# Kernel optimization log

Measured on AMD Instinct MI355X. Metric: run time of the kernel, lower is better.

## Reference

```python
import jax, jax.numpy as jnp
import numpy as np

SIGMA = 32.0
EPS = 1e-8

def setup_inputs() -> dict:
    key = jax.random.key(0)
    k1, k2, k3 = jax.random.split(key, 3)
    N, D, O = 8192, 512, 512
    x = jax.random.normal(k1, (N, D), dtype=jnp.float32)
    # Linear params (kaiming-normal-ish init represented as scaled normals)
    W = jax.random.normal(k2, (O, D), dtype=jnp.float32) * (2.0 / D) ** 0.5
    b = jnp.zeros((O,), dtype=jnp.float32)
    return {"x": x, "W": W, "b": b}

def reference(x, W, b):
    # squared pairwise L2 distances via the Gram trick: ||xi||^2 + ||xj||^2 - 2 xi.xj
    sq = jnp.sum(x * x, axis=-1)                      # [N]
    sqd = sq[:, None] + sq[None, :] - 2.0 * (x @ x.T)  # [N, N]
    sqd = jnp.maximum(sqd, 0.0)                        # numerical clamp (cdist >= 0)
    weights = jnp.exp(-sqd / (2.0 * SIGMA * SIGMA))    # Gaussian kernel [N, N]
    weights = weights / (jnp.sum(weights, axis=1, keepdims=True) + EPS)
    output = weights @ x                               # Nadaraya-Watson weighted avg [N, D]
    return output @ W.T + b                            # linear head [N, O]
```

## Files before the change

kernel.cpp:

```cpp
#include <hip/hip_runtime.h>
#include <stdint.h>

#define NPTS 8192
#define DIM  512
#define ODIM 512

typedef __attribute__((ext_vector_type(8))) short short8;
typedef __attribute__((ext_vector_type(4))) float f32x4;

__device__ __forceinline__ void gload_lds16(const void* g, void* l) {
  __builtin_amdgcn_global_load_lds(
      (__attribute__((address_space(1))) void*)g,
      (__attribute__((address_space(3))) void*)l, 16, 0, 0);
}

__device__ __forceinline__ short f2bf(float f) {
  uint32_t u = __float_as_uint(f);
  u = (u + 0x7FFFu + ((u >> 16) & 1u)) >> 16;
  return (short)u;
}

__device__ __forceinline__ void gemm256_2ph(const short* __restrict__ A,
                                            const short* __restrict__ B,
                                            int K, int lda, int ldb,
                                            short* lds, f32x4 acc[8][4]) {
  const int tid  = threadIdx.x;
  const int wid  = tid >> 6;
  const int lane = tid & 63;
  const int wr = wid >> 2, wc = wid & 3;
  const int fr = lane & 15, fg = lane >> 4;
  const int srow = lane >> 3;
  const int scol = (lane & 7) << 3;

  const short* sa[4];
  const short* sb[4];
  int da[4];
#pragma unroll
  for (int q = 0; q < 4; ++q) {
    const int gi = q * 8 + wid;
    sa[q] = A + (size_t)(gi * 8 + srow) * lda + scol;
    sb[q] = B + (size_t)(gi * 8 + srow) * ldb + scol;
    da[q] = gi * 512;
  }

  auto stage = [&](int bo, int k0) {
#pragma unroll
    for (int q = 0; q < 4; ++q) gload_lds16(sa[q] + k0, lds + bo + da[q]);
#pragma unroll
    for (int q = 0; q < 4; ++q) gload_lds16(sb[q] + k0, lds + bo + 16384 + da[q]);
  };

  auto compute = [&](int bo) {
    const short* sA = lds + bo;
    const short* sB = lds + bo + 16384;
#pragma unroll
    for (int kk = 0; kk < 2; ++kk) {
      short8 af[8], bb[4];
#pragma unroll
      for (int m = 0; m < 8; ++m)
        af[m] = *(const short8*)(sA + (wr * 128 + m * 16 + fr) * 64 + kk * 32 + fg * 8);
#pragma unroll
      for (int n = 0; n < 4; ++n)
        bb[n] = *(const short8*)(sB + (wc * 64 + n * 16 + fr) * 64 + kk * 32 + fg * 8);
#pragma unroll
      for (int m = 0; m < 8; ++m)
#pragma unroll
        for (int n = 0; n < 4; ++n)
          acc[m][n] = __builtin_amdgcn_mfma_f32_16x16x32_bf16(af[m], bb[n], acc[m][n], 0, 0, 0);
    }
  };

  stage(0, 0);
  __syncthreads();
  int bo = 0;
  const int nt = K >> 6;
  for (int t = 0; t < nt - 1; ++t) {
    stage(bo ^ 32768, (t + 1) << 6);
    compute(bo);
    __syncthreads();
    bo ^= 32768;
  }
  compute(bo);
}

#define ZERO_ACC8(acc)                       \
  {                                          \
    f32x4 _z = {0.f, 0.f, 0.f, 0.f};         \
    _Pragma("unroll")                        \
    for (int m = 0; m < 8; ++m)              \
      _Pragma("unroll")                      \
      for (int n = 0; n < 4; ++n) acc[m][n] = _z; \
  }

__device__ __forceinline__ void gemm_core_nt(const short* __restrict__ A,
                                             const short* __restrict__ B,
                                             int K, int lda, int ldb,
                                             short* smem, f32x4 acc[4][4]) {
  const int tid  = threadIdx.x;
  const int wid  = tid >> 6;
  const int lane = tid & 63;
  const int wr = wid >> 1, wc = wid & 1;
  const int sr = lane >> 2;
  const int sc = (lane & 3) << 3;
  const int fr = lane & 15, fg = lane >> 4;
  short* sA = smem;
  short* sB = smem + 4096;
  short* dA0 = sA + wid * 512;
  short* dA1 = sA + 2048 + wid * 512;
  short* dB0 = sB + wid * 512;
  short* dB1 = sB + 2048 + wid * 512;
  const short* pa0 = A + (size_t)(wid * 16 + sr) * lda + sc;
  const short* pa1 = A + (size_t)(64 + wid * 16 + sr) * lda + sc;
  const short* pb0 = B + (size_t)(wid * 16 + sr) * ldb + sc;
  const short* pb1 = B + (size_t)(64 + wid * 16 + sr) * ldb + sc;

  for (int k0 = 0; k0 < K; k0 += 32) {
    gload_lds16(pa0 + k0, dA0);
    gload_lds16(pa1 + k0, dA1);
    gload_lds16(pb0 + k0, dB0);
    gload_lds16(pb1 + k0, dB1);
    __syncthreads();
    short8 af[4], bb[4];
#pragma unroll
    for (int m = 0; m < 4; ++m)
      af[m] = *(const short8*)(sA + (wr * 64 + m * 16 + fr) * 32 + fg * 8);
#pragma unroll
    for (int n = 0; n < 4; ++n)
      bb[n] = *(const short8*)(sB + (wc * 64 + n * 16 + fr) * 32 + fg * 8);
#pragma unroll
    for (int m = 0; m < 4; ++m)
#pragma unroll
      for (int n = 0; n < 4; ++n)
        acc[m][n] = __builtin_amdgcn_mfma_f32_16x16x32_bf16(af[m], bb[n], acc[m][n], 0, 0, 0);
    __syncthreads();
  }
}

#define ZERO_ACC4(acc)                       \
  {                                          \
    f32x4 _z = {0.f, 0.f, 0.f, 0.f};         \
    _Pragma("unroll")                        \
    for (int m = 0; m < 4; ++m)              \
      _Pragma("unroll")                      \
      for (int n = 0; n < 4; ++n) acc[m][n] = _z; \
  }

__global__ __launch_bounds__(256) void k_prep_x(const float* __restrict__ x,
                                                short* __restrict__ xb,
                                                float* __restrict__ sq) {
  const int row  = blockIdx.x * 4 + (threadIdx.x >> 6);
  const int lane = threadIdx.x & 63;
  const float* px = x + (size_t)row * DIM + lane * 8;
  const float4 v0 = *(const float4*)px;
  const float4 v1 = *(const float4*)(px + 4);
  float s = v0.x*v0.x + v0.y*v0.y + v0.z*v0.z + v0.w*v0.w +
            v1.x*v1.x + v1.y*v1.y + v1.z*v1.z + v1.w*v1.w;
  short8 o;
  o[0]=f2bf(v0.x); o[1]=f2bf(v0.y); o[2]=f2bf(v0.z); o[3]=f2bf(v0.w);
  o[4]=f2bf(v1.x); o[5]=f2bf(v1.y); o[6]=f2bf(v1.z); o[7]=f2bf(v1.w);
  *(short8*)(xb + (size_t)row * DIM + lane * 8) = o;
#pragma unroll
  for (int m = 32; m >= 1; m >>= 1) s += __shfl_xor(s, m);
  if (lane == 0) sq[row] = s;
}

__global__ __launch_bounds__(256) void k_prep_w(const float* __restrict__ W,
                                                short* __restrict__ Wb) {
  const int idx = blockIdx.x * 256 + threadIdx.x;
  const float4 v0 = *(const float4*)(W + (size_t)idx * 8);
  const float4 v1 = *(const float4*)(W + (size_t)idx * 8 + 4);
  short8 o;
  o[0]=f2bf(v0.x); o[1]=f2bf(v0.y); o[2]=f2bf(v0.z); o[3]=f2bf(v0.w);
  o[4]=f2bf(v1.x); o[5]=f2bf(v1.y); o[6]=f2bf(v1.z); o[7]=f2bf(v1.w);
  *(short8*)(Wb + (size_t)idx * 8) = o;
}

__global__ __launch_bounds__(256) void k_ybt(const short* __restrict__ xb,
                                             const short* __restrict__ Wb,
                                             short* __restrict__ YbT) {
  __shared__ short smem[8192];
  f32x4 acc[4][4];
  ZERO_ACC4(acc);
  const int rowBase = blockIdx.y * 128;
  const int colBase = blockIdx.x * 128;
  gemm_core_nt(Wb + (size_t)rowBase * DIM, xb + (size_t)colBase * DIM,
               DIM, DIM, DIM, smem, acc);
  const int lane = threadIdx.x & 63, wid = threadIdx.x >> 6;
  const int wr = wid >> 1, wc = wid & 1, fr = lane & 15, fg = lane >> 4;
#pragma unroll
  for (int m = 0; m < 4; ++m)
#pragma unroll
    for (int n = 0; n < 4; ++n)
#pragma unroll
      for (int r = 0; r < 4; ++r) {
        const int ro = rowBase + wr * 64 + m * 16 + fg * 4 + r;
        const int ci = colBase + wc * 64 + n * 16 + fr;
        YbT[(size_t)ro * NPTS + ci] = f2bf(acc[m][n][r]);
      }
}

__global__ __launch_bounds__(512, 2) void k_pmat(const short* __restrict__ xb,
                                                 const float* __restrict__ sq,
                                                 short* __restrict__ P,
                                                 float* __restrict__ rowsum,
                                                 int jbase, int SW) {
  __shared__ short lds[65536];
  f32x4 acc[8][4];
  ZERO_ACC8(acc);
  const int rowBase = blockIdx.y * 256;
  const int colTile = blockIdx.x * 256;
  const int jglob = jbase + colTile;
  gemm256_2ph(xb + (size_t)rowBase * DIM, xb + (size_t)jglob * DIM,
              DIM, DIM, DIM, lds, acc);
  const int lane = threadIdx.x & 63, wid = threadIdx.x >> 6;
  const int wr = wid >> 2, wc = wid & 3, fr = lane & 15, fg = lane >> 4;
  float sj[4];
#pragma unroll
  for (int n = 0; n < 4; ++n) sj[n] = sq[jglob + wc * 64 + n * 16 + fr];
#pragma unroll
  for (int m = 0; m < 8; ++m) {
#pragma unroll
    for (int r = 0; r < 4; ++r) {
      const int i = rowBase + wr * 128 + m * 16 + fg * 4 + r;
      const float si = sq[i];
      float rs = 0.f;
#pragma unroll
      for (int n = 0; n < 4; ++n) {
        const float t = fminf(2.f * acc[m][n][r] - si - sj[n], 0.f) * (1.0f / 2048.0f);
        const float w = __expf(t);
        rs += w;
        P[(size_t)i * SW + (colTile + wc * 64 + n * 16 + fr)] = f2bf(w);
      }
      rs += __shfl_xor(rs, 1);
      rs += __shfl_xor(rs, 2);
      rs += __shfl_xor(rs, 4);
      rs += __shfl_xor(rs, 8);
      if (fr == 0) atomicAdd(&rowsum[i], rs);
    }
  }
}

__global__ __launch_bounds__(512, 2) void k_pv(const short* __restrict__ P,
                                               const short* __restrict__ YbT,
                                               float* __restrict__ out_acc,
                                               int jbase, int SW, int klen) {
  __shared__ short lds[65536];
  f32x4 acc[8][4];
  ZERO_ACC8(acc);
  const int rowBase = blockIdx.y * 256;
  const int colBase = blockIdx.x * 256;
  const int kz = blockIdx.z * klen;
  gemm256_2ph(P + (size_t)rowBase * SW + kz,
              YbT + (size_t)colBase * NPTS + jbase + kz,
              klen, SW, NPTS, lds, acc);
  const int lane = threadIdx.x & 63, wid = threadIdx.x >> 6;
  const int wr = wid >> 2, wc = wid & 3, fr = lane & 15, fg = lane >> 4;
#pragma unroll
  for (int m = 0; m < 8; ++m)
#pragma unroll
    for (int n = 0; n < 4; ++n)
#pragma unroll
      for (int r = 0; r < 4; ++r) {
        const int i = rowBase + wr * 128 + m * 16 + fg * 4 + r;
        const int o = colBase + wc * 64 + n * 16 + fr;
        atomicAdd(&out_acc[(size_t)i * ODIM + o], acc[m][n][r]);
      }
}

__global__ __launch_bounds__(256) void k_final(const float* __restrict__ out_acc,
                                               const float* __restrict__ rowsum,
                                               const float* __restrict__ bvec,
                                               float* __restrict__ out) {
  const int idx = blockIdx.x * 256 + threadIdx.x;
  const int i = idx >> 7;
  const int o = (idx & 127) << 2;
  const float inv = 1.f / (rowsum[i] + 1e-8f);
  const float4 a = *(const float4*)(out_acc + (size_t)i * ODIM + o);
  const float4 bb = *(const float4*)(bvec + o);
  float4 r;
  r.x = a.x * inv + bb.x;
  r.y = a.y * inv + bb.y;
  r.z = a.z * inv + bb.z;
  r.w = a.w * inv + bb.w;
  *(float4*)(out + (size_t)i * ODIM + o) = r;
}

extern "C" void kernel_launch(void* const* d_in, const int* in_sizes, int n_in,
                              void* d_out, int out_size, void* d_ws, size_t ws_size,
                              hipStream_t stream) {
  (void)in_sizes; (void)n_in; (void)out_size;
  const float* x = (const float*)d_in[0];
  const float* W = (const float*)d_in[1];
  const float* bvec = (const float*)d_in[2];
  float* out = (float*)d_out;
  char* ws = (char*)d_ws;

  short* xb      = (short*)(ws + 0);
  short* Wb      = (short*)(ws + 8388608);
  short* YbT     = (short*)(ws + 8912896);
  float* sq      = (float*)(ws + 17301504);
  float* rowsum  = (float*)(ws + 17334272);
  float* out_acc = (float*)(ws + 17367040);
  short* P       = (short*)(ws + 34144256);

  size_t pav = ws_size > 34144256 ? ws_size - 34144256 : 0;
  int SW = 8192;
  while (SW > 256 && (size_t)NPTS * SW * 2 > pav) SW >>= 1;
  const int nstrips = NPTS / SW;
  int ksplit = SW / 2048;
  if (ksplit < 1) ksplit = 1;
  if (ksplit > 4) ksplit = 4;
  const int klen = SW / ksplit;

  hipMemsetAsync(rowsum, 0, NPTS * sizeof(float), stream);
  hipMemsetAsync(out_acc, 0, (size_t)NPTS * ODIM * sizeof(float), stream);

  k_prep_x<<<dim3(NPTS / 4), 256, 0, stream>>>(x, xb, sq);
  k_prep_w<<<dim3(ODIM * DIM / 8 / 256), 256, 0, stream>>>(W, Wb);
  k_ybt<<<dim3(NPTS / 128, ODIM / 128), 256, 0, stream>>>(xb, Wb, YbT);

  for (int s = 0; s < nstrips; ++s) {
    const int jbase = s * SW;
    k_pmat<<<dim3(SW / 256, NPTS / 256), 512, 0, stream>>>(xb, sq, P, rowsum, jbase, SW);
    k_pv<<<dim3(ODIM / 256, NPTS / 256, ksplit), 512, 0, stream>>>(P, YbT, out_acc, jbase, SW, klen);
  }

  k_final<<<dim3(NPTS * ODIM / 4 / 256), 256, 0, stream>>>(out_acc, rowsum, bvec, out);
}
```

Baseline: 360.5 us.

## Deepen GEMM pipeline to four LDS stages with swizzle and XCD block remap

```diff
diff --git a/kernel.cpp b/kernel.cpp
--- a/kernel.cpp
+++ b/kernel.cpp
@@ -20,67 +20,82 @@
   return (short)u;
 }
 
-__device__ __forceinline__ void gemm256_2ph(const short* __restrict__ A,
-                                            const short* __restrict__ B,
-                                            int K, int lda, int ldb,
-                                            short* lds, f32x4 acc[8][4]) {
-  const int tid  = threadIdx.x;
-  const int wid  = tid >> 6;
-  const int lane = tid & 63;
-  const int wr = wid >> 2, wc = wid & 3;
-  const int fr = lane & 15, fg = lane >> 4;
-  const int srow = lane >> 3;
-  const int scol = (lane & 7) << 3;
-
-  const short* sa[4];
-  const short* sb[4];
-  int da[4];
-#pragma unroll
-  for (int q = 0; q < 4; ++q) {
-    const int gi = q * 8 + wid;
-    sa[q] = A + (size_t)(gi * 8 + srow) * lda + scol;
-    sb[q] = B + (size_t)(gi * 8 + srow) * ldb + scol;
-    da[q] = gi * 512;
-  }
-
-  auto stage = [&](int bo, int k0) {
-#pragma unroll
-    for (int q = 0; q < 4; ++q) gload_lds16(sa[q] + k0, lds + bo + da[q]);
-#pragma unroll
-    for (int q = 0; q < 4; ++q) gload_lds16(sb[q] + k0, lds + bo + 16384 + da[q]);
+#define VMB(N) do {                                          \
+    asm volatile("s_waitcnt vmcnt(" #N ")" ::: "memory");    \
+    __builtin_amdgcn_sched_barrier(0);                       \
+    __builtin_amdgcn_s_barrier();                            \
+    __builtin_amdgcn_sched_barrier(0);                       \
+  } while (0)
+
+#define BARRIER_ONLY() do {                                  \
+    asm volatile("" ::: "memory");                           \
+    __builtin_amdgcn_sched_barrier(0);                       \
+    __builtin_amdgcn_s_barrier();                            \
+    __builtin_amdgcn_sched_barrier(0);                       \
+  } while (0)
+
+__device__ __forceinline__ void gemm256_pipe(const short* __restrict__ A,
+                                             const short* __restrict__ B,
+                                             int K, int lda, int ldb,
+                                             short* lds, f32x4 acc[8][4]) {
+  const int tid = threadIdx.x, wid = tid >> 6, lane = tid & 63;
+  const int wr = wid >> 2, wc = wid & 3, fr = lane & 15, fg = (lane >> 4) & 3;
+  const int nt = K >> 5;
+
+  const short* ga[2]; const short* gb[2]; int dl[2];
+#pragma unroll
+  for (int s = 0; s < 2; ++s) {
+    const int row = (wid * 2 + s) * 16 + (lane >> 2);
+    const int ch  = (lane & 3) ^ ((row & 3) ^ ((row >> 2) & 3));
+    ga[s] = A + (size_t)row * lda + ch * 8;
+    gb[s] = B + (size_t)row * ldb + ch * 8;
+    dl[s] = (wid * 2 + s) * 512;
+  }
+  auto stage = [&](int t) {
+    short* slot = lds + (t & 3) * 16384;
+    const int k0 = t << 5;
+#pragma unroll
+    for (int s = 0; s < 2; ++s) gload_lds16(ga[s] + k0, slot + dl[s]);
+#pragma unroll
+    for (int s = 0; s < 2; ++s) gload_lds16(gb[s] + k0, slot + 8192 + dl[s]);
   };
 
-  auto compute = [&](int bo) {
-    const short* sA = lds + bo;
-    const short* sB = lds + bo + 16384;
-#pragma unroll
-    for (int kk = 0; kk < 2; ++kk) {
-      short8 af[8], bb[4];
-#pragma unroll
-      for (int m = 0; m < 8; ++m)
-        af[m] = *(const short8*)(sA + (wr * 128 + m * 16 + fr) * 64 + kk * 32 + fg * 8);
+  auto compute = [&](int t) {
+    const short* sA = lds + (t & 3) * 16384;
+    const short* sB = sA + 8192;
+    short8 af[8], bb[4];
+#pragma unroll
+    for (int m = 0; m < 8; ++m) {
+      const int r = wr * 128 + m * 16 + fr;
+      const int c = fg ^ ((r & 3) ^ ((r >> 2) & 3));
+      af[m] = *(const short8*)(sA + r * 32 + c * 8);
+    }
+#pragma unroll
+    for (int n = 0; n < 4; ++n) {
+      const int r = wc * 64 + n * 16 + fr;
+      const int c = fg ^ ((r & 3) ^ ((r >> 2) & 3));
+      bb[n] = *(const short8*)(sB + r * 32 + c * 8);
+    }
+    __builtin_amdgcn_s_setprio(1);
+#pragma unroll
+    for (int m = 0; m < 8; ++m)
 #pragma unroll
       for (int n = 0; n < 4; ++n)
-        bb[n] = *(const short8*)(sB + (wc * 64 + n * 16 + fr) * 64 + kk * 32 + fg * 8);
-#pragma unroll
-      for (int m = 0; m < 8; ++m)
-#pragma unroll
-        for (int n = 0; n < 4; ++n)
-          acc[m][n] = __builtin_amdgcn_mfma_f32_16x16x32_bf16(af[m], bb[n], acc[m][n], 0, 0, 0);
-    }
+        acc[m][n] = __builtin_amdgcn_mfma_f32_16x16x32_bf16(af[m], bb[n], acc[m][n], 0, 0, 0);
+    __builtin_amdgcn_s_setprio(0);
   };
 
-  stage(0, 0);
-  __syncthreads();
-  int bo = 0;
-  const int nt = K >> 6;
-  for (int t = 0; t < nt - 1; ++t) {
-    stage(bo ^ 32768, (t + 1) << 6);
-    compute(bo);
-    __syncthreads();
-    bo ^= 32768;
-  }
-  compute(bo);
+  stage(0); stage(1); stage(2);
+  for (int t = 0; t < nt; ++t) {
+    if (t + 3 < nt) stage(t + 3);
+    const int rem = nt - 1 - t;
+    if (rem >= 3)      VMB(12);
+    else if (rem == 2) VMB(8);
+    else if (rem == 1) VMB(4);
+    else               VMB(0);
+    compute(t);
+    BARRIER_ONLY();
+  }
 }
 
 #define ZERO_ACC8(acc)                       \
@@ -91,6 +106,16 @@
       _Pragma("unroll")                      \
       for (int n = 0; n < 4; ++n) acc[m][n] = _z; \
   }
+
+__device__ __forceinline__ void xcd_swizzle(int& bx, int& by) {
+  const int gx = gridDim.x, nxy = gx * gridDim.y;
+  int orig = by * gx + bx;
+  if ((nxy & 7) == 0) {
+    const int cpx = nxy >> 3;
+    orig = (orig & 7) * cpx + (orig >> 3);
+  }
+  bx = orig % gx; by = orig / gx;
+}
 
 __device__ __forceinline__ void gemm_core_nt(const short* __restrict__ A,
                                              const short* __restrict__ B,
@@ -207,11 +232,13 @@
   __shared__ short lds[65536];
   f32x4 acc[8][4];
   ZERO_ACC8(acc);
-  const int rowBase = blockIdx.y * 256;
-  const int colTile = blockIdx.x * 256;
+  int bx = blockIdx.x, by = blockIdx.y;
+  xcd_swizzle(bx, by);
+  const int rowBase = by * 256;
+  const int colTile = bx * 256;
   const int jglob = jbase + colTile;
-  gemm256_2ph(xb + (size_t)rowBase * DIM, xb + (size_t)jglob * DIM,
-              DIM, DIM, DIM, lds, acc);
+  gemm256_pipe(xb + (size_t)rowBase * DIM, xb + (size_t)jglob * DIM,
+               DIM, DIM, DIM, lds, acc);
   const int lane = threadIdx.x & 63, wid = threadIdx.x >> 6;
   const int wr = wid >> 2, wc = wid & 3, fr = lane & 15, fg = lane >> 4;
   float sj[4];
@@ -247,12 +274,14 @@
   __shared__ short lds[65536];
   f32x4 acc[8][4];
   ZERO_ACC8(acc);
-  const int rowBase = blockIdx.y * 256;
-  const int colBase = blockIdx.x * 256;
+  int bx = blockIdx.x, by = blockIdx.y;
+  xcd_swizzle(bx, by);
+  const int rowBase = by * 256;
+  const int colBase = bx * 256;
   const int kz = blockIdx.z * klen;
-  gemm256_2ph(P + (size_t)rowBase * SW + kz,
-              YbT + (size_t)colBase * NPTS + jbase + kz,
-              klen, SW, NPTS, lds, acc);
+  gemm256_pipe(P + (size_t)rowBase * SW + kz,
+               YbT + (size_t)colBase * NPTS + jbase + kz,
+               klen, SW, NPTS, lds, acc);
   const int lane = threadIdx.x & 63, wid = threadIdx.x >> 6;
   const int wr = wid >> 2, wc = wid & 3, fr = lane & 15, fg = lane >> 4;
 #pragma unroll
```

Result: slower. 380.1 us (+5.4%).
